# Performance work log

Hardware: AMD Instinct MI355X
Metric: run time of the kernel (lower is better)

Reference implementation:

```python
import jax, jax.numpy as jnp
import numpy as np
from jax import lax

NUM_CLUSTER = 128
N_ITERS = 10


def setup_inputs() -> dict:
    key = jax.random.key(0)
    feat_g = jax.random.normal(key, (131072, 256), dtype=jnp.float32)
    return {"feat_g": feat_g}


def _sq_dists(x, c):
    x2 = jnp.sum(x * x, axis=1, keepdims=True)            # [N,1]
    c2 = jnp.sum(c * c, axis=1)                           # [K]
    return x2 - 2.0 * (x @ c.T) + c2[None, :]


def _kmeans_fit(x, k, iters):
    n = x.shape[0]
    init_c = x[:k]  # deterministic init: first k points
    ones = jnp.ones((n,), dtype=x.dtype)

    def step(c, _):
        assign = jnp.argmin(_sq_dists(x, c), axis=1)                 # [N]
        sums = jax.ops.segment_sum(x, assign, num_segments=k)       # [K,d]
        counts = jax.ops.segment_sum(ones, assign, num_segments=k)  # [K]
        new_c = sums / jnp.maximum(counts, 1.0)[:, None]
        new_c = jnp.where(counts[:, None] > 0, new_c, c)  # keep empty clusters
        return new_c, None

    c, _ = lax.scan(step, init_c, None, length=iters)
    return c


def reference(feat_g):
    # view(batch, -1, dim) then view(-1, dim) is an identity reshape for the math
    x = lax.stop_gradient(feat_g)  # original detaches feat_gc before fit/predict
    c = _kmeans_fit(x, NUM_CLUSTER, N_ITERS)
    preds = jnp.argmin(_sq_dists(x, c), axis=1)  # [N] int labels
    return preds
```

## Files before the change

kernel.cpp:

```cpp
#include <hip/hip_runtime.h>

#define NPTS 131072
#define DIM 256
#define NK 128
#define NITER 10
#define SEG 16
#define SLICES 64
#define PTS_PER_SLICE (NPTS / SLICES)

typedef _Float16 half8 __attribute__((ext_vector_type(8)));
typedef _Float16 half4v __attribute__((ext_vector_type(4)));
typedef float f32x4 __attribute__((ext_vector_type(4)));

#define RSCALE 4096.0f
#define RINV 2.44140625e-4f

__global__ void x2_kernel(const float* __restrict__ x, float* __restrict__ x2) {
  int tid = threadIdx.x;
  int p = blockIdx.x * 16 + (tid >> 4);
  int part = tid & 15;
  const float4* xr = (const float4*)(x + (size_t)p * DIM);
  float s = 0.f;
#pragma unroll
  for (int j = 0; j < 4; ++j) {
    float4 v = xr[part * 4 + j];
    s += v.x * v.x;
    s += v.y * v.y;
    s += v.z * v.z;
    s += v.w * v.w;
  }
#pragma unroll
  for (int m = 8; m >= 1; m >>= 1) s += __shfl_xor(s, m, 16);
  if (part == 0) x2[p] = s;
}

__global__ void c2_kernel(const float* __restrict__ c, float* __restrict__ c2) {
  int k = blockIdx.x, lane = threadIdx.x;
  float4 v = ((const float4*)(c + (size_t)k * DIM))[lane];
  float s = v.x * v.x + v.y * v.y + v.z * v.z + v.w * v.w;
#pragma unroll
  for (int m = 32; m >= 1; m >>= 1) s += __shfl_xor(s, m, 64);
  if (lane == 0) c2[k] = s;
}

__global__ void convert_x2_kernel(const float* __restrict__ x, _Float16* __restrict__ x1,
                                  _Float16* __restrict__ x2s, float* __restrict__ x2) {
  int tid = threadIdx.x;
  int p = blockIdx.x * 16 + (tid >> 4);
  int part = tid & 15;
  const float4* xr = (const float4*)(x + (size_t)p * DIM);
  half4v* o1 = (half4v*)(x1 + (size_t)p * DIM);
  half4v* o2 = (half4v*)(x2s + (size_t)p * DIM);
  float s = 0.f;
#pragma unroll
  for (int j = 0; j < 4; ++j) {
    float4 v = xr[part * 4 + j];
    float f[4] = {v.x, v.y, v.z, v.w};
    half4v h, l;
#pragma unroll
    for (int u = 0; u < 4; ++u) {
      _Float16 hi = (_Float16)f[u];
      float r = f[u] - (float)hi;
      h[u] = hi;
      l[u] = (_Float16)(r * RSCALE);
      s += f[u] * f[u];
    }
    o1[part * 4 + j] = h;
    o2[part * 4 + j] = l;
  }
#pragma unroll
  for (int m = 8; m >= 1; m >>= 1) s += __shfl_xor(s, m, 16);
  if (part == 0) x2[p] = s;
}

__global__ void convert_c_kernel(const float* __restrict__ c, _Float16* __restrict__ ct) {
  int i = blockIdx.x * 256 + threadIdx.x;
  int k = i >> 6;
  int d4 = i & 63;
  float4 v = ((const float4*)c)[i];
  float f[4] = {v.x, v.y, v.z, v.w};
  half4v h, l;
#pragma unroll
  for (int j = 0; j < 4; ++j) {
    _Float16 hi = (_Float16)f[j];
    float r = f[j] - (float)hi;
    h[j] = hi;
    l[j] = (_Float16)(r * RSCALE);
  }
  int ch = d4 >> 3;
  int idx4 = ch * 2048 + k * 8 + (d4 & 7);
  ((half4v*)ct)[idx4] = h;
  ((half4v*)ct)[idx4 + 1024] = l;
}

template <bool DOHIST>
__global__ __launch_bounds__(256, 2) void assign_mfma_kernel(
    const _Float16* __restrict__ x1, const _Float16* __restrict__ x2s,
    const _Float16* __restrict__ ct, const float* __restrict__ x2,
    const float* __restrict__ c2, int* __restrict__ out, int* __restrict__ counts) {
  __shared__ __align__(16) _Float16 cbuf[2][8192];
  __shared__ int hcnt[NK];

  int tid = threadIdx.x;
  int lane = tid & 63;
  int w = tid >> 6;
  int lcol = lane & 15;
  int lgrp = lane >> 4;
  int row0 = blockIdx.x * 128 + w * 32;

  if (DOHIST && tid < NK) hcnt[tid] = 0;

  const _Float16* xa = x1 + (size_t)(row0 + lcol) * DIM + lgrp * 8;
  const _Float16* xb = x2s + (size_t)(row0 + lcol) * DIM + lgrp * 8;
  const half8* ctv = (const half8*)ct;

  f32x4 acc1[2][8], acc2[2][8];
#pragma unroll
  for (int rt = 0; rt < 2; ++rt)
#pragma unroll
    for (int c8 = 0; c8 < 8; ++c8) {
      acc1[rt][c8] = f32x4{0.f, 0.f, 0.f, 0.f};
      acc2[rt][c8] = f32x4{0.f, 0.f, 0.f, 0.f};
    }

  half8 A1[2], A2[2], nA1[2], nA2[2], sreg[4];

#pragma unroll
  for (int r = 0; r < 4; ++r) sreg[r] = ctv[r * 256 + tid];
#pragma unroll
  for (int rt = 0; rt < 2; ++rt) {
    A1[rt] = *(const half8*)(xa + rt * 16 * DIM);
    A2[rt] = *(const half8*)(xb + rt * 16 * DIM);
  }
#pragma unroll
  for (int r = 0; r < 4; ++r) ((half8*)cbuf[0])[r * 256 + tid] = sreg[r];
  __syncthreads();

#pragma unroll
  for (int ck = 0; ck < 8; ++ck) {
    const int cb = ck & 1;
    if (ck < 7) {
#pragma unroll
      for (int r = 0; r < 4; ++r) sreg[r] = ctv[(ck + 1) * 1024 + r * 256 + tid];
#pragma unroll
      for (int rt = 0; rt < 2; ++rt) {
        nA1[rt] = *(const half8*)(xa + rt * 16 * DIM + (ck + 1) * 32);
        nA2[rt] = *(const half8*)(xb + rt * 16 * DIM + (ck + 1) * 32);
      }
    }
#pragma unroll
    for (int c8 = 0; c8 < 8; ++c8) {
      int bidx = (c8 * 16 + lcol) * 32 + lgrp * 8;
      half8 b1 = *(const half8*)&cbuf[cb][bidx];
      half8 b2 = *(const half8*)&cbuf[cb][4096 + bidx];
#pragma unroll
      for (int rt = 0; rt < 2; ++rt) {
        acc1[rt][c8] = __builtin_amdgcn_mfma_f32_16x16x32_f16(A1[rt], b1, acc1[rt][c8], 0, 0, 0);
        acc2[rt][c8] = __builtin_amdgcn_mfma_f32_16x16x32_f16(A1[rt], b2, acc2[rt][c8], 0, 0, 0);
        acc2[rt][c8] = __builtin_amdgcn_mfma_f32_16x16x32_f16(A2[rt], b1, acc2[rt][c8], 0, 0, 0);
      }
    }
    if (ck < 7) {
#pragma unroll
      for (int r = 0; r < 4; ++r) ((half8*)cbuf[cb ^ 1])[r * 256 + tid] = sreg[r];
#pragma unroll
      for (int rt = 0; rt < 2; ++rt) {
        A1[rt] = nA1[rt];
        A2[rt] = nA2[rt];
      }
      __syncthreads();
    }
  }

#pragma unroll
  for (int rt = 0; rt < 2; ++rt) {
    int pbase = row0 + rt * 16 + lgrp * 4;
    float x2p[4];
#pragma unroll
    for (int r = 0; r < 4; ++r) x2p[r] = x2[pbase + r];
    float bv[4];
    int bk[4];
#pragma unroll
    for (int r = 0; r < 4; ++r) { bv[r] = 3.4e38f; bk[r] = 0; }
#pragma unroll
    for (int c8 = 0; c8 < 8; ++c8) {
      int kc = c8 * 16 + lcol;
      float c2k = c2[kc];
#pragma unroll
      for (int r = 0; r < 4; ++r) {
        float dot = fmaf(acc2[rt][c8][r], RINV, acc1[rt][c8][r]);
        float d = fmaf(-2.f, dot, x2p[r]) + c2k;
        if (d < bv[r]) { bv[r] = d; bk[r] = kc; }
      }
    }
#pragma unroll
    for (int m = 1; m <= 8; m <<= 1) {
#pragma unroll
      for (int r = 0; r < 4; ++r) {
        float ov = __shfl_xor(bv[r], m, 64);
        int ok = __shfl_xor(bk[r], m, 64);
        if (ov < bv[r] || (ov == bv[r] && ok < bk[r])) { bv[r] = ov; bk[r] = ok; }
      }
    }
    if (lcol == 0) {
#pragma unroll
      for (int r = 0; r < 4; ++r) {
        out[pbase + r] = bk[r];
        if (DOHIST) atomicAdd(&hcnt[bk[r]], 1);
      }
    }
  }

  if (DOHIST) {
    __syncthreads();
    if (tid < NK) {
      int v = hcnt[tid];
      if (v) atomicAdd(&counts[tid], v);
    }
  }
}

__global__ __launch_bounds__(256, 2) void csum_kernel(
    const _Float16* __restrict__ x1, const _Float16* __restrict__ x2s,
    const int* __restrict__ assignb, float* __restrict__ p1, float* __restrict__ p2) {
  __shared__ __align__(16) _Float16 bt[2][2][32][40];
  __shared__ int abuf[2][32];

  int tid = threadIdx.x;
  int lane = tid & 63;
  int w = tid >> 6;
  int slice = blockIdx.x;
  int d0 = blockIdx.y * 32;
  int ibase = slice * PTS_PER_SLICE;
  int kbase = w * 32;
  int lcol = lane & 15;
  int lgrp = lane >> 4;

  int sarr = tid >> 7;
  int srow = (tid >> 2) & 31;
  int scs = tid & 3;
  const _Float16* xsrc = sarr ? x2s : x1;

  f32x4 acc1[2][2], acc2[2][2];
#pragma unroll
  for (int kt = 0; kt < 2; ++kt)
#pragma unroll
    for (int dt = 0; dt < 2; ++dt) {
      acc1[kt][dt] = f32x4{0.f, 0.f, 0.f, 0.f};
      acc2[kt][dt] = f32x4{0.f, 0.f, 0.f, 0.f};
    }

  {
    half8 v = *(const half8*)(xsrc + (size_t)(ibase + srow) * DIM + d0 + scs * 8);
#pragma unroll
    for (int j = 0; j < 8; ++j) bt[0][sarr][scs * 8 + j][srow] = v[j];
    if (tid < 8) ((int4*)abuf[0])[tid] = ((const int4*)(assignb + ibase))[tid];
  }
  __syncthreads();

  for (int ci = 0; ci < PTS_PER_SLICE / 32; ++ci) {
    const int cb = ci & 1;
    half8 nv;
    int4 na;
    if (ci < PTS_PER_SLICE / 32 - 1) {
      int i0 = ibase + (ci + 1) * 32;
      nv = *(const half8*)(xsrc + (size_t)(i0 + srow) * DIM + d0 + scs * 8);
      if (tid < 8) na = ((const int4*)(assignb + i0))[tid];
    }

    int4 av0 = ((int4*)abuf[cb])[lgrp * 2];
    int4 av1 = ((int4*)abuf[cb])[lgrp * 2 + 1];
    int aj[8] = {av0.x, av0.y, av0.z, av0.w, av1.x, av1.y, av1.z, av1.w};
    half8 oh[2];
#pragma unroll
    for (int kt = 0; kt < 2; ++kt) {
      int kk = kbase + kt * 16 + lcol;
#pragma unroll
      for (int j = 0; j < 8; ++j) oh[kt][j] = (aj[j] == kk) ? (_Float16)1.0f : (_Float16)0.0f;
    }
#pragma unroll
    for (int dt = 0; dt < 2; ++dt) {
      half8 b1 = *(const half8*)&bt[cb][0][dt * 16 + lcol][lgrp * 8];
      half8 b2 = *(const half8*)&bt[cb][1][dt * 16 + lcol][lgrp * 8];
#pragma unroll
      for (int kt = 0; kt < 2; ++kt) {
        acc1[kt][dt] = __builtin_amdgcn_mfma_f32_16x16x32_f16(oh[kt], b1, acc1[kt][dt], 0, 0, 0);
        acc2[kt][dt] = __builtin_amdgcn_mfma_f32_16x16x32_f16(oh[kt], b2, acc2[kt][dt], 0, 0, 0);
      }
    }

    if (ci < PTS_PER_SLICE / 32 - 1) {
      __syncthreads();
#pragma unroll
      for (int j = 0; j < 8; ++j) bt[cb ^ 1][sarr][scs * 8 + j][srow] = nv[j];
      if (tid < 8) ((int4*)abuf[cb ^ 1])[tid] = na;
      __syncthreads();
    }
  }

#pragma unroll
  for (int kt = 0; kt < 2; ++kt)
#pragma unroll
    for (int dt = 0; dt < 2; ++dt) {
      int dd = d0 + dt * 16 + lcol;
#pragma unroll
      for (int r = 0; r < 4; ++r) {
        int krow = kbase + kt * 16 + lgrp * 4 + r;
        size_t idx = ((size_t)slice * NK + krow) * DIM + dd;
        p1[idx] = acc1[kt][dt][r];
        p2[idx] = acc2[kt][dt][r];
      }
    }
}

__global__ void reduce_v3_kernel(const float* __restrict__ p1, const float* __restrict__ p2,
                                 int* __restrict__ counts, float* __restrict__ c,
                                 float* __restrict__ c2, _Float16* __restrict__ ct) {
  __shared__ float wsum[4];
  int k = blockIdx.x, d = threadIdx.x;
  int cnt = counts[k];
  float s1 = 0.f, s2v = 0.f;
#pragma unroll 4
  for (int s = 0; s < SLICES; ++s) {
    size_t idx = ((size_t)s * NK + k) * DIM + d;
    s1 += p1[idx];
    s2v += p2[idx];
  }
  float s = fmaf(s2v, RINV, s1);

  float nc;
  if (cnt > 0)
    nc = s / fmaxf((float)cnt, 1.0f);
  else
    nc = c[(size_t)k * DIM + d];
  c[(size_t)k * DIM + d] = nc;

  {
    _Float16 hi = (_Float16)nc;
    float r = nc - (float)hi;
    _Float16 lov = (_Float16)(r * RSCALE);
    int ch = d >> 5, dd = d & 31;
    ct[ch * 8192 + k * 32 + dd] = hi;
    ct[ch * 8192 + k * 32 + dd + 4096] = lov;
  }

  float sq = nc * nc;
#pragma unroll
  for (int m = 32; m >= 1; m >>= 1) sq += __shfl_xor(sq, m, 64);
  if ((threadIdx.x & 63) == 0) wsum[threadIdx.x >> 6] = sq;
  __syncthreads();
  if (threadIdx.x == 0) {
    c2[k] = wsum[0] + wsum[1] + wsum[2] + wsum[3];
    counts[k] = 0;
  }
}

__global__ void assign_kernel(const float* __restrict__ x, const float* __restrict__ c,
                              const float* __restrict__ x2, const float* __restrict__ c2,
                              int* __restrict__ assign_out) {
  __shared__ float4 xs4[64 * 4];
  __shared__ float4 cs4[128 * 4];
  __shared__ float redv[64][17];
  __shared__ int redk[64][17];

  int tid = threadIdx.x;
  int tx = tid & 15;
  int ty = tid >> 4;
  int row0 = blockIdx.x * 64;

  float acc[4][8];
#pragma unroll
  for (int a = 0; a < 4; ++a)
#pragma unroll
    for (int b = 0; b < 8; ++b) acc[a][b] = 0.f;

  for (int ck = 0; ck < 16; ++ck) {
    {
      int p = tid >> 2, d4 = tid & 3;
      float4 v = *(const float4*)(x + (size_t)(row0 + p) * DIM + ck * 16 + d4 * 4);
      xs4[p * 4 + (d4 ^ ((p >> 2) & 3))] = v;
    }
#pragma unroll
    for (int r = 0; r < 2; ++r) {
      int idx = tid + r * 256;
      int kk = idx >> 2, dd = idx & 3;
      float4 v = *(const float4*)(c + (size_t)kk * DIM + ck * 16 + dd * 4);
      cs4[kk * 4 + (dd ^ ((kk >> 3) & 3))] = v;
    }
    __syncthreads();
#pragma unroll
    for (int d4 = 0; d4 < 4; ++d4) {
      float4 xr[4], cr[8];
#pragma unroll
      for (int pp = 0; pp < 4; ++pp) xr[pp] = xs4[(tx * 4 + pp) * 4 + (d4 ^ (tx & 3))];
#pragma unroll
      for (int kk = 0; kk < 8; ++kk) cr[kk] = cs4[(ty * 8 + kk) * 4 + (d4 ^ (ty & 3))];
#pragma unroll
      for (int pp = 0; pp < 4; ++pp)
#pragma unroll
        for (int kk = 0; kk < 8; ++kk) {
          acc[pp][kk] = fmaf(xr[pp].x, cr[kk].x, acc[pp][kk]);
          acc[pp][kk] = fmaf(xr[pp].y, cr[kk].y, acc[pp][kk]);
          acc[pp][kk] = fmaf(xr[pp].z, cr[kk].z, acc[pp][kk]);
          acc[pp][kk] = fmaf(xr[pp].w, cr[kk].w, acc[pp][kk]);
        }
    }
    __syncthreads();
  }

  float x2p[4];
#pragma unroll
  for (int pp = 0; pp < 4; ++pp) x2p[pp] = x2[row0 + tx * 4 + pp];

  float bestv[4];
  int bestk[4];
#pragma unroll
  for (int pp = 0; pp < 4; ++pp) { bestv[pp] = 3.4e38f; bestk[pp] = 0; }
#pragma unroll
  for (int kk = 0; kk < 8; ++kk) {
    float c2k = c2[ty * 8 + kk];
#pragma unroll
    for (int pp = 0; pp < 4; ++pp) {
      float d = fmaf(-2.f, acc[pp][kk], x2p[pp]) + c2k;
      if (d < bestv[pp]) { bestv[pp] = d; bestk[pp] = ty * 8 + kk; }
    }
  }
#pragma unroll
  for (int pp = 0; pp < 4; ++pp) {
    redv[tx * 4 + pp][ty] = bestv[pp];
    redk[tx * 4 + pp][ty] = bestk[pp];
  }
  __syncthreads();
  if (tid < 64) {
    float bv = redv[tid][0];
    int bk = redk[tid][0];
#pragma unroll
    for (int t = 1; t < 16; ++t) {
      float v = redv[tid][t];
      if (v < bv) { bv = v; bk = redk[tid][t]; }
    }
    assign_out[row0 + tid] = bk;
  }
}

__global__ void hist_kernel(const int* __restrict__ assign_in, int* __restrict__ hist) {
  __shared__ int h[NK];
  int tid = threadIdx.x, b = blockIdx.x;
  if (tid < NK) h[tid] = 0;
  __syncthreads();
#pragma unroll
  for (int r = 0; r < 4; ++r) {
    int a = assign_in[b * 1024 + r * 256 + tid];
    atomicAdd(&h[a], 1);
  }
  __syncthreads();
  if (tid < NK) hist[b * NK + tid] = h[tid];
}

__global__ void scan_fb_kernel(const int* __restrict__ hist, int* __restrict__ base,
                               int* __restrict__ counts, int* __restrict__ cbase) {
  __shared__ int h[128 * NK];
  int tid = threadIdx.x;
  for (int i = tid; i < 128 * NK; i += 256) h[i] = hist[i];
  __syncthreads();
  if (tid < NK) {
    int run = 0;
    for (int b = 0; b < 128; ++b) {
      int v = h[b * NK + tid];
      h[b * NK + tid] = run;
      run += v;
    }
    counts[tid] = run;
  }
  __syncthreads();
  if (tid == 0) {
    int cb = 0;
    for (int j = 0; j < NK; ++j) {
      cbase[j] = cb;
      cb += counts[j];
    }
  }
  __syncthreads();
  if (tid < NK) {
    int cbk = cbase[tid];
    for (int b = 0; b < 128; ++b) base[b * NK + tid] = h[b * NK + tid] + cbk;
  }
}

__global__ void scatter_kernel(const int* __restrict__ assign_in, const int* __restrict__ base,
                               int* __restrict__ perm) {
  __shared__ int cnt[NK];
  int lane = threadIdx.x, b = blockIdx.x;
  cnt[lane] = base[b * NK + lane];
  cnt[lane + 64] = base[b * NK + lane + 64];
  for (int r = 0; r < 16; ++r) {
    int p = b * 1024 + r * 64 + lane;
    int a = assign_in[p];
    unsigned long long mask = ~0ull;
#pragma unroll
    for (int j = 0; j < 7; ++j) {
      unsigned long long bal = __ballot((a >> j) & 1);
      mask &= ((a >> j) & 1) ? bal : ~bal;
    }
    int rank = __popcll(mask & ((1ull << lane) - 1ull));
    int pos = cnt[a] + rank;
    perm[pos] = p;
    if (rank == 0) cnt[a] += (int)__popcll(mask);
  }
}

__global__ void seg_sum_kernel(const float* __restrict__ x, const int* __restrict__ perm,
                               const int* __restrict__ counts, const int* __restrict__ cbase,
                               float* __restrict__ partial) {
  int k = blockIdx.x, s = blockIdx.y, d = threadIdx.x;
  int cnt = counts[k], off = cbase[k];
  int j0 = (int)(((long long)cnt * s) / SEG);
  int j1 = (int)(((long long)cnt * (s + 1)) / SEG);
  float sum = 0.f;
  int j = j0;
  for (; j + 4 <= j1; j += 4) {
    int p0 = perm[off + j + 0];
    int p1 = perm[off + j + 1];
    int p2 = perm[off + j + 2];
    int p3 = perm[off + j + 3];
    sum += x[(size_t)p0 * DIM + d];
    sum += x[(size_t)p1 * DIM + d];
    sum += x[(size_t)p2 * DIM + d];
    sum += x[(size_t)p3 * DIM + d];
  }
  for (; j < j1; ++j) sum += x[(size_t)perm[off + j] * DIM + d];
  partial[((size_t)k * SEG + s) * DIM + d] = sum;
}

__global__ void reduce_fb_kernel(const float* __restrict__ partial, const int* __restrict__ counts,
                                 float* __restrict__ c, float* __restrict__ c2) {
  __shared__ float wsum[4];
  int k = blockIdx.x, d = threadIdx.x;
  int cnt = counts[k];
  float s = 0.f;
#pragma unroll
  for (int t = 0; t < SEG; ++t) s += partial[((size_t)k * SEG + t) * DIM + d];
  float nc;
  if (cnt > 0)
    nc = s / fmaxf((float)cnt, 1.0f);
  else
    nc = c[(size_t)k * DIM + d];
  c[(size_t)k * DIM + d] = nc;
  float s2 = nc * nc;
#pragma unroll
  for (int m = 32; m >= 1; m >>= 1) s2 += __shfl_xor(s2, m, 64);
  if ((threadIdx.x & 63) == 0) wsum[threadIdx.x >> 6] = s2;
  __syncthreads();
  if (threadIdx.x == 0) c2[k] = wsum[0] + wsum[1] + wsum[2] + wsum[3];
}

extern "C" void kernel_launch(void* const* d_in, const int* in_sizes, int n_in,
                              void* d_out, int out_size, void* d_ws, size_t ws_size,
                              hipStream_t stream) {
  const float* x = (const float*)d_in[0];
  char* ws = (char*)d_ws;

  const size_t NEED_BIG = 152306688;
  bool use_mfma = ws_size >= NEED_BIG;

  if (use_mfma) {
    _Float16* x1 = (_Float16*)(ws + 0);
    _Float16* x2s = (_Float16*)(ws + 67108864);
    float* c = (float*)(ws + 134217728);
    _Float16* ct = (_Float16*)(ws + 134348800);
    float* c2 = (float*)(ws + 134479872);
    float* x2 = (float*)(ws + 134480384);
    int* assignb = (int*)(ws + 135004672);
    int* counts = (int*)(ws + 135528960);
    float* p1 = (float*)(ws + 135529472);
    float* p2 = (float*)(ws + 143918080);

    hipMemcpyAsync(c, x, (size_t)NK * DIM * sizeof(float), hipMemcpyDeviceToDevice, stream);
    hipMemsetAsync(counts, 0, NK * sizeof(int), stream);
    convert_x2_kernel<<<NPTS / 16, 256, 0, stream>>>(x, x1, x2s, x2);
    c2_kernel<<<NK, 64, 0, stream>>>(c, c2);
    convert_c_kernel<<<NK * DIM / 4 / 256, 256, 0, stream>>>(c, ct);

    for (int it = 0; it < NITER; ++it) {
      assign_mfma_kernel<true>
          <<<NPTS / 128, 256, 0, stream>>>(x1, x2s, ct, x2, c2, assignb, counts);
      csum_kernel<<<dim3(SLICES, DIM / 32), 256, 0, stream>>>(x1, x2s, assignb, p1, p2);
      reduce_v3_kernel<<<NK, 256, 0, stream>>>(p1, p2, counts, c, c2, ct);
    }
    assign_mfma_kernel<false>
        <<<NPTS / 128, 256, 0, stream>>>(x1, x2s, ct, x2, c2, (int*)d_out, counts);
  } else {
    float* c = (float*)(ws + 0);
    float* c2 = (float*)(ws + 131072);
    float* x2 = (float*)(ws + 132096);
    int* assignb = (int*)(ws + 656384);
    int* hist = (int*)(ws + 1180672);
    int* base = (int*)(ws + 1246208);
    int* counts = (int*)(ws + 1311744);
    int* cbase = (int*)(ws + 1312256);
    int* perm = (int*)(ws + 1312768);
    float* partial = (float*)(ws + 1837056);

    hipMemcpyAsync(c, x, (size_t)NK * DIM * sizeof(float), hipMemcpyDeviceToDevice, stream);
    x2_kernel<<<NPTS / 16, 256, 0, stream>>>(x, x2);
    c2_kernel<<<NK, 64, 0, stream>>>(c, c2);

    for (int it = 0; it < NITER; ++it) {
      assign_kernel<<<NPTS / 64, 256, 0, stream>>>(x, c, x2, c2, assignb);
      hist_kernel<<<NPTS / 1024, 256, 0, stream>>>(assignb, hist);
      scan_fb_kernel<<<1, 256, 0, stream>>>(hist, base, counts, cbase);
      scatter_kernel<<<NPTS / 1024, 64, 0, stream>>>(assignb, base, perm);
      seg_sum_kernel<<<dim3(NK, SEG), 256, 0, stream>>>(x, perm, counts, cbase, partial);
      reduce_fb_kernel<<<NK, 256, 0, stream>>>(partial, counts, c, c2);
    }
    assign_kernel<<<NPTS / 64, 256, 0, stream>>>(x, c, x2, c2, (int*)d_out);
  }
}
```

Before: 1.092 ms.

## Enlarge csum chunk to 128 points and merge hi/lo partials before reduce

The centroid-sum kernel now stages 128 points per double-buffered chunk instead of 32, so each barrier pair covers four MFMA k-steps and each thread loads four contiguous 16-byte vectors per row. The hi and lo partial sums are combined in the csum epilogue, so only one partial buffer is written and the reduce kernel reads half as much. The x conversion kernel also writes 16-byte vectors instead of 8-byte ones. The trade-off is more shared memory per block and more registers for the prefetched chunk, which could lower occupancy. The transposed LDS stores may also hit more bank conflicts.

```diff
diff --git a/kernel.cpp b/kernel.cpp
--- a/kernel.cpp
+++ b/kernel.cpp
@@ -7,6 +7,7 @@
 #define SEG 16
 #define SLICES 64
 #define PTS_PER_SLICE (NPTS / SLICES)
+#define CHUNK 128
 
 typedef _Float16 half8 __attribute__((ext_vector_type(8)));
 typedef _Float16 half4v __attribute__((ext_vector_type(4)));
@@ -49,24 +50,27 @@
   int p = blockIdx.x * 16 + (tid >> 4);
   int part = tid & 15;
   const float4* xr = (const float4*)(x + (size_t)p * DIM);
-  half4v* o1 = (half4v*)(x1 + (size_t)p * DIM);
-  half4v* o2 = (half4v*)(x2s + (size_t)p * DIM);
+  half8* o1 = (half8*)(x1 + (size_t)p * DIM);
+  half8* o2 = (half8*)(x2s + (size_t)p * DIM);
   float s = 0.f;
+  half8 hh[2], ll[2];
 #pragma unroll
   for (int j = 0; j < 4; ++j) {
     float4 v = xr[part * 4 + j];
     float f[4] = {v.x, v.y, v.z, v.w};
-    half4v h, l;
 #pragma unroll
     for (int u = 0; u < 4; ++u) {
       _Float16 hi = (_Float16)f[u];
       float r = f[u] - (float)hi;
-      h[u] = hi;
-      l[u] = (_Float16)(r * RSCALE);
+      hh[j >> 1][(j & 1) * 4 + u] = hi;
+      ll[j >> 1][(j & 1) * 4 + u] = (_Float16)(r * RSCALE);
       s += f[u] * f[u];
     }
-    o1[part * 4 + j] = h;
-    o2[part * 4 + j] = l;
+  }
+#pragma unroll
+  for (int jj = 0; jj < 2; ++jj) {
+    o1[part * 2 + jj] = hh[jj];
+    o2[part * 2 + jj] = ll[jj];
   }
 #pragma unroll
   for (int m = 8; m >= 1; m >>= 1) s += __shfl_xor(s, m, 16);
@@ -222,9 +226,9 @@
 
 __global__ __launch_bounds__(256, 2) void csum_kernel(
     const _Float16* __restrict__ x1, const _Float16* __restrict__ x2s,
-    const int* __restrict__ assignb, float* __restrict__ p1, float* __restrict__ p2) {
-  __shared__ __align__(16) _Float16 bt[2][2][32][40];
-  __shared__ int abuf[2][32];
+    const int* __restrict__ assignb, float* __restrict__ p) {
+  __shared__ __align__(16) _Float16 bt[2][2][32][136];
+  __shared__ int abuf[2][CHUNK];
 
   int tid = threadIdx.x;
   int lane = tid & 63;
@@ -237,8 +241,7 @@
   int lgrp = lane >> 4;
 
   int sarr = tid >> 7;
-  int srow = (tid >> 2) & 31;
-  int scs = tid & 3;
+  int srow = tid & 127;
   const _Float16* xsrc = sarr ? x2s : x1;
 
   f32x4 acc1[2][2], acc2[2][2];
@@ -251,49 +254,63 @@
     }
 
   {
-    half8 v = *(const half8*)(xsrc + (size_t)(ibase + srow) * DIM + d0 + scs * 8);
-#pragma unroll
-    for (int j = 0; j < 8; ++j) bt[0][sarr][scs * 8 + j][srow] = v[j];
-    if (tid < 8) ((int4*)abuf[0])[tid] = ((const int4*)(assignb + ibase))[tid];
-  }
-  __syncthreads();
-
-  for (int ci = 0; ci < PTS_PER_SLICE / 32; ++ci) {
+    const half8* src = (const half8*)(xsrc + (size_t)(ibase + srow) * DIM + d0);
+    half8 v[4];
+#pragma unroll
+    for (int q = 0; q < 4; ++q) v[q] = src[q];
+#pragma unroll
+    for (int q = 0; q < 4; ++q)
+#pragma unroll
+      for (int j = 0; j < 8; ++j) bt[0][sarr][q * 8 + j][srow] = v[q][j];
+    if (tid < 32) ((int4*)abuf[0])[tid] = ((const int4*)(assignb + ibase))[tid];
+  }
+  __syncthreads();
+
+  const int NCH = PTS_PER_SLICE / CHUNK;
+  for (int ci = 0; ci < NCH; ++ci) {
     const int cb = ci & 1;
-    half8 nv;
+    half8 nv[4];
     int4 na;
-    if (ci < PTS_PER_SLICE / 32 - 1) {
-      int i0 = ibase + (ci + 1) * 32;
-      nv = *(const half8*)(xsrc + (size_t)(i0 + srow) * DIM + d0 + scs * 8);
-      if (tid < 8) na = ((const int4*)(assignb + i0))[tid];
-    }
-
-    int4 av0 = ((int4*)abuf[cb])[lgrp * 2];
-    int4 av1 = ((int4*)abuf[cb])[lgrp * 2 + 1];
-    int aj[8] = {av0.x, av0.y, av0.z, av0.w, av1.x, av1.y, av1.z, av1.w};
-    half8 oh[2];
-#pragma unroll
-    for (int kt = 0; kt < 2; ++kt) {
-      int kk = kbase + kt * 16 + lcol;
-#pragma unroll
-      for (int j = 0; j < 8; ++j) oh[kt][j] = (aj[j] == kk) ? (_Float16)1.0f : (_Float16)0.0f;
-    }
-#pragma unroll
-    for (int dt = 0; dt < 2; ++dt) {
-      half8 b1 = *(const half8*)&bt[cb][0][dt * 16 + lcol][lgrp * 8];
-      half8 b2 = *(const half8*)&bt[cb][1][dt * 16 + lcol][lgrp * 8];
+    bool more = (ci < NCH - 1);
+    if (more) {
+      const half8* src =
+          (const half8*)(xsrc + (size_t)(ibase + (ci + 1) * CHUNK + srow) * DIM + d0);
+#pragma unroll
+      for (int q = 0; q < 4; ++q) nv[q] = src[q];
+      if (tid < 32) na = ((const int4*)(assignb + ibase + (ci + 1) * CHUNK))[tid];
+    }
+
+#pragma unroll
+    for (int ks = 0; ks < 4; ++ks) {
+      int4 av0 = ((int4*)abuf[cb])[ks * 8 + lgrp * 2];
+      int4 av1 = ((int4*)abuf[cb])[ks * 8 + lgrp * 2 + 1];
+      int aj[8] = {av0.x, av0.y, av0.z, av0.w, av1.x, av1.y, av1.z, av1.w};
+      half8 oh[2];
 #pragma unroll
       for (int kt = 0; kt < 2; ++kt) {
-        acc1[kt][dt] = __builtin_amdgcn_mfma_f32_16x16x32_f16(oh[kt], b1, acc1[kt][dt], 0, 0, 0);
-        acc2[kt][dt] = __builtin_amdgcn_mfma_f32_16x16x32_f16(oh[kt], b2, acc2[kt][dt], 0, 0, 0);
-      }
-    }
-
-    if (ci < PTS_PER_SLICE / 32 - 1) {
+        int kk = kbase + kt * 16 + lcol;
+#pragma unroll
+        for (int j = 0; j < 8; ++j) oh[kt][j] = (aj[j] == kk) ? (_Float16)1.0f : (_Float16)0.0f;
+      }
+#pragma unroll
+      for (int dt = 0; dt < 2; ++dt) {
+        half8 b1 = *(const half8*)&bt[cb][0][dt * 16 + lcol][ks * 32 + lgrp * 8];
+        half8 b2 = *(const half8*)&bt[cb][1][dt * 16 + lcol][ks * 32 + lgrp * 8];
+#pragma unroll
+        for (int kt = 0; kt < 2; ++kt) {
+          acc1[kt][dt] = __builtin_amdgcn_mfma_f32_16x16x32_f16(oh[kt], b1, acc1[kt][dt], 0, 0, 0);
+          acc2[kt][dt] = __builtin_amdgcn_mfma_f32_16x16x32_f16(oh[kt], b2, acc2[kt][dt], 0, 0, 0);
+        }
+      }
+    }
+
+    if (more) {
       __syncthreads();
 #pragma unroll
-      for (int j = 0; j < 8; ++j) bt[cb ^ 1][sarr][scs * 8 + j][srow] = nv[j];
-      if (tid < 8) ((int4*)abuf[cb ^ 1])[tid] = na;
+      for (int q = 0; q < 4; ++q)
+#pragma unroll
+        for (int j = 0; j < 8; ++j) bt[cb ^ 1][sarr][q * 8 + j][srow] = nv[q][j];
+      if (tid < 32) ((int4*)abuf[cb ^ 1])[tid] = na;
       __syncthreads();
     }
   }
@@ -306,27 +323,21 @@
 #pragma unroll
       for (int r = 0; r < 4; ++r) {
         int krow = kbase + kt * 16 + lgrp * 4 + r;
-        size_t idx = ((size_t)slice * NK + krow) * DIM + dd;
-        p1[idx] = acc1[kt][dt][r];
-        p2[idx] = acc2[kt][dt][r];
-      }
-    }
-}
-
-__global__ void reduce_v3_kernel(const float* __restrict__ p1, const float* __restrict__ p2,
-                                 int* __restrict__ counts, float* __restrict__ c,
-                                 float* __restrict__ c2, _Float16* __restrict__ ct) {
+        p[((size_t)slice * NK + krow) * DIM + dd] =
+            fmaf(acc2[kt][dt][r], RINV, acc1[kt][dt][r]);
+      }
+    }
+}
+
+__global__ void reduce_v4_kernel(const float* __restrict__ p, int* __restrict__ counts,
+                                 float* __restrict__ c, float* __restrict__ c2,
+                                 _Float16* __restrict__ ct) {
   __shared__ float wsum[4];
   int k = blockIdx.x, d = threadIdx.x;
   int cnt = counts[k];
-  float s1 = 0.f, s2v = 0.f;
+  float s = 0.f;
 #pragma unroll 4
-  for (int s = 0; s < SLICES; ++s) {
-    size_t idx = ((size_t)s * NK + k) * DIM + d;
-    s1 += p1[idx];
-    s2v += p2[idx];
-  }
-  float s = fmaf(s2v, RINV, s1);
+  for (int sl = 0; sl < SLICES; ++sl) s += p[((size_t)sl * NK + k) * DIM + d];
 
   float nc;
   if (cnt > 0)
@@ -560,7 +571,7 @@
   const float* x = (const float*)d_in[0];
   char* ws = (char*)d_ws;
 
-  const size_t NEED_BIG = 152306688;
+  const size_t NEED_BIG = 143918080;
   bool use_mfma = ws_size >= NEED_BIG;
 
   if (use_mfma) {
@@ -572,8 +583,7 @@
     float* x2 = (float*)(ws + 134480384);
     int* assignb = (int*)(ws + 135004672);
     int* counts = (int*)(ws + 135528960);
-    float* p1 = (float*)(ws + 135529472);
-    float* p2 = (float*)(ws + 143918080);
+    float* p = (float*)(ws + 135529472);
 
     hipMemcpyAsync(c, x, (size_t)NK * DIM * sizeof(float), hipMemcpyDeviceToDevice, stream);
     hipMemsetAsync(counts, 0, NK * sizeof(int), stream);
@@ -584,8 +594,8 @@
     for (int it = 0; it < NITER; ++it) {
       assign_mfma_kernel<true>
           <<<NPTS / 128, 256, 0, stream>>>(x1, x2s, ct, x2, c2, assignb, counts);
-      csum_kernel<<<dim3(SLICES, DIM / 32), 256, 0, stream>>>(x1, x2s, assignb, p1, p2);
-      reduce_v3_kernel<<<NK, 256, 0, stream>>>(p1, p2, counts, c, c2, ct);
+      csum_kernel<<<dim3(SLICES, DIM / 32), 256, 0, stream>>>(x1, x2s, assignb, p);
+      reduce_v4_kernel<<<NK, 256, 0, stream>>>(p, counts, c, c2, ct);
     }
     assign_mfma_kernel<false>
         <<<NPTS / 128, 256, 0, stream>>>(x1, x2s, ct, x2, c2, (int*)d_out, counts);
```

Result: faster. 1.002 ms (-8.3%).
